# Performance work log

Hardware: AMD Instinct MI355X
Metric: run time of the kernel (lower is better)

The kernel has to match this reference:

```python
import jax, jax.numpy as jnp
import numpy as np

EPS = 1e-12


def pairwise_sqdist(x, y):
    # x: (B, N, 3), y: (B, M, 3) -> (B, N, M) squared euclidean distances
    xx = jnp.sum(x * x, axis=-1)              # (B, N)
    yy = jnp.sum(y * y, axis=-1)              # (B, M)
    xy = jnp.einsum('bnd,bmd->bnm', x, y)     # (B, N, M)
    d = xx[:, :, None] + yy[None_ if False else yy[:, None, :].shape and 0 or ...] if False else xx[:, :, None] + yy[:, None, :] - 2.0 * xy
    return jnp.maximum(d, 0.0)


def chamfer_l1(x, y):
    # pytorch3d/PoinTr-style ChamferDistanceL1:
    # mean over points of sqrt(min squared dist), averaged over both directions
    d = pairwise_sqdist(x, y)                 # (B, N, M)
    d1 = jnp.min(d, axis=2)                   # (B, N) x -> nearest y
    d2 = jnp.min(d, axis=1)                   # (B, M) y -> nearest x
    d1 = jnp.sqrt(jnp.maximum(d1, EPS))
    d2 = jnp.sqrt(jnp.maximum(d2, EPS))
    return 0.5 * (jnp.mean(d1) + jnp.mean(d2))


def knn1_gather(x, y):
    # For each point in x (B,N,3), find nearest neighbor in y (B,M,3) (K=1)
    # and gather it -> (B, N, 3). Matches knn_points + knn_gather + squeeze.
    d = pairwise_sqdist(x, y)                 # (B, N, M)
    idx = jnp.argmin(d, axis=2)               # (B, N) int
    return jnp.take_along_axis(y, idx[:, :, None], axis=1)  # (B, N, 3)


def volume_with_wedge(p):
    # wedge-product volume over consecutive point triples:
    # V = sum_i (p_i x p_{i+1}) . p_{i+2} / 6  -> (B,)
    c = jnp.cross(p[:, :-2, :], p[:, 1:-1, :])  # (B, N-2, 3)
    return jnp.sum(jnp.einsum('bnd,bnd->bn', c, p[:, 2:, :]), axis=-1) / 6.0


def setup_inputs() -> dict:
    key = jax.random.key(0)
    k1, k2, k3 = jax.random.split(key, 3)
    B, Nc, Nf, M = 2, 512, 8192, 8192
    return {
        'source_coarse': jax.random.normal(k1, (B, Nc, 3), dtype=jnp.float32),
        'source_fine': jax.random.normal(k2, (B, Nf, 3), dtype=jnp.float32),
        'target_points': jax.random.normal(k3, (B, M, 3), dtype=jnp.float32),
    }


def reference(source_coarse, source_fine, target_points):
    lambda_rot = lambda_ref = lambda_align = lambda_geo = 1.0
    B = source_fine.shape[0]
    axis = jnp.broadcast_to(jnp.array([0.0, 0.0, 1.0], dtype=source_fine.dtype), (B, 3))
    plane_normal = jnp.broadcast_to(jnp.array([0.0, 1.0, 0.0], dtype=source_fine.dtype), (B, 3))

    # KNN (K=1) gather of nearest target point for each fine source point
    new_target = knn1_gather(source_fine, target_points)  # (B, Nf, 3)

    # alignment (Chamfer L1) losses
    loss_align_coarse = chamfer_l1(source_coarse, target_points)
    loss_align_fine = chamfer_l1(source_fine, target_points)

    # rotational symmetry loss
    in_proj = jnp.einsum('bij,bj->bi', source_fine, axis)      # (B, Nf)
    re_proj = jnp.einsum('bij,bj->bi', new_target, axis)
    loss_rot = jnp.mean((jnp.linalg.norm(in_proj, axis=-1) - jnp.linalg.norm(re_proj, axis=-1)) ** 2)

    # reflectional symmetry loss
    pn = plane_normal / jnp.linalg.norm(plane_normal, axis=-1, keepdims=True)
    in_dist = jnp.einsum('bij,bj->bi', source_fine, pn)
    re_dist = jnp.einsum('bij,bj->bi', new_target, pn)
    loss_ref = jnp.mean((in_dist - re_dist) ** 2)

    # geometric consistency (wedge-product volume) loss
    loss_geo = jnp.mean((volume_with_wedge(source_fine) - volume_with_wedge(new_target)) ** 2)

    total = (lambda_rot * loss_rot + lambda_ref * loss_ref
             + lambda_align * loss_align_coarse + lambda_align * loss_align_fine
             + lambda_geo * loss_geo)
    return total
```

## Files before the change

kernel.cpp:

```cpp
#include <hip/hip_runtime.h>
#include <stdint.h>
#include <float.h>

using u64 = unsigned long long;
typedef float v2f __attribute__((ext_vector_type(2)));

constexpr int B_ = 2;
constexpr int NC = 512;
constexpr int NF = 8192;
constexpr int MT = 8192;

constexpr int TPB  = 256;
constexpr int RPB  = 512;
constexpr int TILE = 256;
constexpr int CF   = 16;
constexpr int TAIL_BLOCKS = 196;

#define DEVINL __device__ __forceinline__

template<bool ARGMIN, int R2>
DEVINL void pairmin_body(const float* __restrict__ P, const float* __restrict__ Q,
                         int nP, int nQ, int b, int row_base, int j0, int ntiles,
                         int chunk, int nRowsTot,
                         u64* __restrict__ outPack, unsigned* __restrict__ outVal,
                         float4* tile)
{
#pragma clang fp contract(off)
    const int tid = threadIdx.x;
    v2f tx0[R2], tx1[R2], tx2[R2], txx[R2], dbest[R2];
    int jb[2 * R2];
    #pragma unroll
    for (int r = 0; r < R2; ++r) {
        const int row0 = row_base + tid + (2 * r) * TPB;
        const int row1 = row_base + tid + (2 * r + 1) * TPB;
        const float* p0 = P + ((size_t)b * nP + row0) * 3;
        const float* p1 = P + ((size_t)b * nP + row1) * 3;
        float a0 = p0[0], a1 = p0[1], a2 = p0[2];
        float e0 = p1[0], e1 = p1[1], e2 = p1[2];
        tx0[r] = v2f{2.0f * a0, 2.0f * e0};
        tx1[r] = v2f{2.0f * a1, 2.0f * e1};
        tx2[r] = v2f{2.0f * a2, 2.0f * e2};
        txx[r] = v2f{(a0*a0 + a1*a1) + a2*a2, (e0*e0 + e1*e1) + e2*e2};
        dbest[r] = v2f{FLT_MAX, FLT_MAX};
        jb[2 * r] = 0; jb[2 * r + 1] = 0;
    }

    auto PROC = [&](const float4 qv, const int j) {
#pragma clang fp contract(off)
        #pragma unroll
        for (int r = 0; r < R2; ++r) {
            v2f s = (tx0[r] * qv.x + tx1[r] * qv.y) + tx2[r] * qv.z;
            v2f d = (txx[r] + qv.w) - s;
            if (ARGMIN) {
                bool c0 = d.x < dbest[r].x;
                bool c1 = d.y < dbest[r].y;
                dbest[r] = __builtin_elementwise_min(d, dbest[r]);
                jb[2 * r]     = c0 ? j : jb[2 * r];
                jb[2 * r + 1] = c1 ? j : jb[2 * r + 1];
            } else {
                dbest[r] = __builtin_elementwise_min(dbest[r], d);
            }
        }
    };

    {
        const float* q = Q + ((size_t)b * nQ + j0 + tid) * 3;
        float nq0 = q[0], nq1 = q[1], nq2 = q[2];

        for (int t = 0; t < ntiles; ++t) {
            __syncthreads();
            tile[tid] = make_float4(nq0, nq1, nq2, (nq0*nq0 + nq1*nq1) + nq2*nq2);
            if (t + 1 < ntiles) {
                const float* qn = Q + ((size_t)b * nQ + j0 + (t + 1) * TILE + tid) * 3;
                nq0 = qn[0]; nq1 = qn[1]; nq2 = qn[2];
            }
            __syncthreads();
            const int jbase = j0 + t * TILE;

            float4 qa[4], qb[4];
            #pragma unroll
            for (int u = 0; u < 4; ++u) qa[u] = tile[u];

            for (int jj = 0; jj < TILE; jj += 8) {
                #pragma unroll
                for (int u = 0; u < 4; ++u) qb[u] = tile[jj + 4 + u];
                #pragma unroll
                for (int u = 0; u < 4; ++u) PROC(qa[u], jbase + jj + u);
                #pragma unroll
                for (int u = 0; u < 4; ++u) qa[u] = tile[(jj + 8 + u) & (TILE - 1)];
                #pragma unroll
                for (int u = 0; u < 4; ++u) PROC(qb[u], jbase + jj + 4 + u);
            }
        }
    }

    const v2f vzero = {0.0f, 0.0f};
    const size_t o0 = (size_t)chunk * nRowsTot + (size_t)b * nP;
    #pragma unroll
    for (int r = 0; r < R2; ++r) {
        v2f dcl = __builtin_elementwise_max(dbest[r], vzero);
        const int row0 = row_base + tid + (2 * r) * TPB;
        const int row1 = row_base + tid + (2 * r + 1) * TPB;
        if (ARGMIN) {
            outPack[o0 + row0] = ((u64)__float_as_uint(dcl.x) << 32) | (unsigned)jb[2 * r];
            outPack[o0 + row1] = ((u64)__float_as_uint(dcl.y) << 32) | (unsigned)jb[2 * r + 1];
        } else {
            outVal[o0 + row0] = __float_as_uint(dcl.x);
            outVal[o0 + row1] = __float_as_uint(dcl.y);
        }
    }
}

__global__ __launch_bounds__(TPB, 4) void pairmin_all(
    const float* __restrict__ coarse, const float* __restrict__ fine,
    const float* __restrict__ tgt,
    u64* __restrict__ pfr, unsigned* __restrict__ pfc,
    unsigned* __restrict__ pcr, unsigned* __restrict__ pcc,
    unsigned* __restrict__ counter)
{
    __shared__ float4 tile[TILE];
    const int bx = blockIdx.x;
    if (bx == 0 && threadIdx.x == 0) *counter = 0;
    if (bx < 256) {
        int chunk = bx & 15, yb = (bx >> 4) & 7, b = bx >> 7;
        pairmin_body<true, 2>(fine, tgt, NF, MT, b, yb * 1024, chunk * (MT / CF), 2,
                              chunk, B_ * NF, pfr, nullptr, tile);
    } else if (bx < 512) {
        int i = bx - 256;
        int chunk = i & 15, yb = (i >> 4) & 7, b = i >> 7;
        pairmin_body<false, 2>(tgt, fine, MT, NF, b, yb * 1024, chunk * (NF / CF), 2,
                               chunk, B_ * MT, nullptr, pfc, tile);
    } else if (bx < 576) {
        int i = bx - 512;
        int chunk = i & 31, b = i >> 5;
        pairmin_body<false, 1>(coarse, tgt, NC, MT, b, 0, chunk * TILE, 1,
                               chunk, B_ * NC, nullptr, pcr, tile);
    } else {
        int i = bx - 576;
        int chunk = i & 1, yb = (i >> 1) & 15, b = i >> 5;
        pairmin_body<false, 1>(tgt, coarse, MT, NC, b, yb * RPB, chunk * TILE, 1,
                               chunk, B_ * MT, nullptr, pcc, tile);
    }
}

__global__ __launch_bounds__(TPB) void tail_all(
    const float* __restrict__ fine, const float* __restrict__ tgt,
    const u64* __restrict__ pfr, const unsigned* __restrict__ pfc,
    const unsigned* __restrict__ pcr, const unsigned* __restrict__ pcc,
    double* __restrict__ bs, unsigned* __restrict__ counter,
    float* __restrict__ out)
{
    __shared__ float sp[TPB + 2][3], yp[TPB + 2][3];
    __shared__ double redw[4][9];
    __shared__ double lred[4][13];
    __shared__ int lastflag;
    const int bx = blockIdx.x, tid = threadIdx.x;
    const int wave = tid >> 6, lane = tid & 63;

    double v_s = 0, v_d2f = 0, v_d1c = 0, v_d2c = 0, v_yd2 = 0, v_zs = 0, v_zt = 0;
    double vs = 0, vt = 0;
    int role_b = 0;

    if (bx < 64) {
        const int base = bx * TPB;
        const int g = base + tid;
        const int b = base >> 13;  role_b = b;
        u64 best = pfr[g];
        #pragma unroll
        for (int c = 1; c < CF; ++c) {
            u64 p = pfr[(size_t)c * (B_ * NF) + g];
            best = p < best ? p : best;
        }
        float d1 = __uint_as_float((unsigned)(best >> 32));
        int idx  = (int)(best & 0xffffffffULL);
        float s = sqrtf(fmaxf(d1, 1e-12f));
        const float* y  = tgt  + ((size_t)b * MT + idx) * 3;
        const float* sr = fine + (size_t)g * 3;
        float y0 = y[0],  y1 = y[1],  y2 = y[2];
        float s0 = sr[0], s1 = sr[1], s2 = sr[2];
        yp[tid][0] = y0; yp[tid][1] = y1; yp[tid][2] = y2;
        sp[tid][0] = s0; sp[tid][1] = s1; sp[tid][2] = s2;
        const int base_b = base & (NF - 1);
        if (tid < 2 && base_b + TPB + tid < NF) {
            int g2 = base + TPB + tid;
            u64 b2 = pfr[g2];
            #pragma unroll
            for (int c = 1; c < CF; ++c) {
                u64 p = pfr[(size_t)c * (B_ * NF) + g2];
                b2 = p < b2 ? p : b2;
            }
            int i2 = (int)(b2 & 0xffffffffULL);
            const float* yh = tgt  + ((size_t)b * MT + i2) * 3;
            const float* sh = fine + (size_t)g2 * 3;
            #pragma unroll
            for (int k = 0; k < 3; ++k) { yp[TPB + tid][k] = yh[k]; sp[TPB + tid][k] = sh[k]; }
        }
        __syncthreads();
        v_s = s;
        float yd = s1 - y1;
        v_yd2 = (double)(yd * yd);
        v_zs  = (double)(s2 * s2);
        v_zt  = (double)(y2 * y2);
        int rb = base_b + tid;
        if (rb <= NF - 3) {
            {
                const float* a = sp[tid]; const float* c = sp[tid+1]; const float* e = sp[tid+2];
                float c0 = a[1]*c[2] - a[2]*c[1];
                float c1 = a[2]*c[0] - a[0]*c[2];
                float c2 = a[0]*c[1] - a[1]*c[0];
                vs = (double)(c0*e[0] + c1*e[1] + c2*e[2]);
            }
            {
                const float* a = yp[tid]; const float* c = yp[tid+1]; const float* e = yp[tid+2];
                float c0 = a[1]*c[2] - a[2]*c[1];
                float c1 = a[2]*c[0] - a[0]*c[2];
                float c2 = a[0]*c[1] - a[1]*c[0];
                vt = (double)(c0*e[0] + c1*e[1] + c2*e[2]);
            }
        }
    } else if (bx < 128) {
        const int g = (bx - 64) * TPB + tid;
        unsigned best = pfc[g];
        #pragma unroll
        for (int c = 1; c < CF; ++c) best = min(best, pfc[(size_t)c * (B_ * MT) + g]);
        v_d2f = (double)sqrtf(fmaxf(__uint_as_float(best), 1e-12f));
    } else if (bx < 132) {
        const int g = (bx - 128) * TPB + tid;
        unsigned best = pcr[g];
        #pragma unroll
        for (int c = 1; c < 32; ++c) best = min(best, pcr[(size_t)c * (B_ * NC) + g]);
        v_d1c = (double)sqrtf(fmaxf(__uint_as_float(best), 1e-12f));
    } else {
        const int g = (bx - 132) * TPB + tid;
        unsigned best = min(pcc[g], pcc[(size_t)(B_ * MT) + g]);
        v_d2c = (double)sqrtf(fmaxf(__uint_as_float(best), 1e-12f));
    }

    double r9[9] = {v_s, v_d2f, v_d1c, v_d2c, v_yd2, v_zs, v_zt, vs, vt};
    for (int o = 32; o; o >>= 1) {
        #pragma unroll
        for (int k = 0; k < 9; ++k) r9[k] += __shfl_down(r9[k], o);
    }
    if (lane == 0) {
        #pragma unroll
        for (int k = 0; k < 9; ++k) redw[wave][k] = r9[k];
    }
    __syncthreads();
    if (tid == 0) {
        double t9[9];
        #pragma unroll
        for (int k = 0; k < 9; ++k)
            t9[k] = redw[0][k] + redw[1][k] + redw[2][k] + redw[3][k];
        double* o = bs + (size_t)bx * 16;
        #pragma unroll
        for (int k = 0; k < 16; ++k) o[k] = 0.0;
        o[0] = t9[0]; o[1] = t9[1]; o[2] = t9[2]; o[3] = t9[3]; o[4] = t9[4];
        o[5 + role_b]  = t9[5];
        o[7 + role_b]  = t9[6];
        o[9 + role_b]  = t9[7];
        o[11 + role_b] = t9[8];
        __threadfence();
        unsigned old = atomicAdd(counter, 1u);
        lastflag = (old == TAIL_BLOCKS - 1);
    }
    __syncthreads();
    if (!lastflag) return;

    __threadfence();
    double c13[13];
    if (tid < TAIL_BLOCKS) {
        const double* p = bs + (size_t)tid * 16;
        #pragma unroll
        for (int k = 0; k < 13; ++k) c13[k] = p[k];
    } else {
        #pragma unroll
        for (int k = 0; k < 13; ++k) c13[k] = 0.0;
    }
    for (int o = 32; o; o >>= 1) {
        #pragma unroll
        for (int k = 0; k < 13; ++k) c13[k] += __shfl_down(c13[k], o);
    }
    if (lane == 0) {
        #pragma unroll
        for (int k = 0; k < 13; ++k) lred[wave][k] = c13[k];
    }
    __syncthreads();
    if (tid == 0) {
        double S[13];
        #pragma unroll
        for (int k = 0; k < 13; ++k)
            S[k] = lred[0][k] + lred[1][k] + lred[2][k] + lred[3][k];
        double m_d1f = S[0] / (double)(B_ * NF);
        double m_d2f = S[1] / (double)(B_ * MT);
        double m_d1c = S[2] / (double)(B_ * NC);
        double m_d2c = S[3] / (double)(B_ * MT);
        double loss_align_fine   = 0.5 * (m_d1f + m_d2f);
        double loss_align_coarse = 0.5 * (m_d1c + m_d2c);
        double loss_ref = S[4] / (double)(B_ * NF);
        double loss_rot = 0.0, loss_geo = 0.0;
        for (int b = 0; b < B_; ++b) {
            double dn = sqrt(S[5 + b]) - sqrt(S[7 + b]);
            loss_rot += dn * dn;
            double dv = (S[9 + b] - S[11 + b]) / 6.0;
            loss_geo += dv * dv;
        }
        loss_rot /= (double)B_;
        loss_geo /= (double)B_;
        out[0] = (float)(loss_rot + loss_ref + loss_align_coarse + loss_align_fine + loss_geo);
    }
}

extern "C" void kernel_launch(void* const* d_in, const int* in_sizes, int n_in,
                              void* d_out, int out_size, void* d_ws, size_t ws_size,
                              hipStream_t stream)
{
    const float* src_coarse = (const float*)d_in[0];
    const float* src_fine   = (const float*)d_in[1];
    const float* tgt        = (const float*)d_in[2];
    float* out = (float*)d_out;
    char*  ws  = (char*)d_ws;

    u64*      pfr     = (u64*)(ws);
    unsigned* pfc     = (unsigned*)(ws + 2097152);
    unsigned* pcr     = (unsigned*)(ws + 3145728);
    unsigned* pcc     = (unsigned*)(ws + 3276800);
    double*   bs      = (double*)(ws + 3407872);
    unsigned* counter = (unsigned*)(ws + 3432960);

    pairmin_all<<<dim3(640), TPB, 0, stream>>>(
        src_coarse, src_fine, tgt, pfr, pfc, pcr, pcc, counter);
    tail_all<<<dim3(TAIL_BLOCKS), TPB, 0, stream>>>(
        src_fine, tgt, pfr, pfc, pcr, pcc, bs, counter, out);
}
```

Before: 117.5 us.

## Broadcast query points via readlane instead of LDS tiles and rebalance block work

Replaces the shared-memory tile of query points with per-wave register loading, using readlane to broadcast each point's coordinates across the wave. This removes __syncthreads and LDS traffic from the inner distance loop. Every block now runs both fine-direction phases plus one coarse phase, with the work split into more chunks (32/128/8), so the workspace and tail reductions grow. The scalar broadcasts may occupy the SALU and limit issue rate, and the argmin update changes from a vector min to per-lane selects.

After: 124.8 us. +6.2%, slower.

```diff
diff --git a/kernel.cpp b/kernel.cpp
--- a/kernel.cpp
+++ b/kernel.cpp
@@ -10,23 +10,28 @@
 constexpr int NF = 8192;
 constexpr int MT = 8192;
 
-constexpr int TPB  = 256;
-constexpr int RPB  = 512;
-constexpr int TILE = 256;
-constexpr int CF   = 16;
+constexpr int TPB = 256;
+constexpr int CFF = 32;
+constexpr int CCR = 128;
+constexpr int CCC = 8;
 constexpr int TAIL_BLOCKS = 196;
 
 #define DEVINL __device__ __forceinline__
 
+DEVINL float bcast(float v, int l) {
+    return __int_as_float(__builtin_amdgcn_readlane(__float_as_int(v), l));
+}
+
 template<bool ARGMIN, int R2>
-DEVINL void pairmin_body(const float* __restrict__ P, const float* __restrict__ Q,
-                         int nP, int nQ, int b, int row_base, int j0, int ntiles,
-                         int chunk, int nRowsTot,
-                         u64* __restrict__ outPack, unsigned* __restrict__ outVal,
-                         float4* tile)
+DEVINL void pairmin_phase(const float* __restrict__ P, const float* __restrict__ Q,
+                          int nP, int nQ, int b, int row_base, int j0, int ntiles,
+                          int chunk, int nRowsTot,
+                          u64* __restrict__ outPack, unsigned* __restrict__ outVal)
 {
 #pragma clang fp contract(off)
-    const int tid = threadIdx.x;
+    const int tid  = threadIdx.x;
+    const int lane = tid & 63;
+
     v2f tx0[R2], tx1[R2], tx2[R2], txx[R2], dbest[R2];
     int jb[2 * R2];
     #pragma unroll
@@ -45,53 +50,39 @@
         jb[2 * r] = 0; jb[2 * r + 1] = 0;
     }
 
-    auto PROC = [&](const float4 qv, const int j) {
-#pragma clang fp contract(off)
-        #pragma unroll
-        for (int r = 0; r < R2; ++r) {
-            v2f s = (tx0[r] * qv.x + tx1[r] * qv.y) + tx2[r] * qv.z;
-            v2f d = (txx[r] + qv.w) - s;
-            if (ARGMIN) {
-                bool c0 = d.x < dbest[r].x;
-                bool c1 = d.y < dbest[r].y;
-                dbest[r] = __builtin_elementwise_min(d, dbest[r]);
-                jb[2 * r]     = c0 ? j : jb[2 * r];
-                jb[2 * r + 1] = c1 ? j : jb[2 * r + 1];
-            } else {
-                dbest[r] = __builtin_elementwise_min(dbest[r], d);
+    const float* qp = Q + ((size_t)b * nQ + j0 + lane) * 3;
+    float cq0 = qp[0], cq1 = qp[1], cq2 = qp[2];
+
+    for (int t = 0; t < ntiles; ++t) {
+        float cqq = (cq0*cq0 + cq1*cq1) + cq2*cq2;
+        const int t2 = (t + 1 < ntiles) ? t + 1 : t;
+        const float* qn = Q + ((size_t)b * nQ + j0 + t2 * 64 + lane) * 3;
+        float nq0 = qn[0], nq1 = qn[1], nq2 = qn[2];
+        const int jbase = j0 + t * 64;
+
+        #pragma unroll
+        for (int l = 0; l < 64; ++l) {
+            const float q0 = bcast(cq0, l);
+            const float q1 = bcast(cq1, l);
+            const float q2 = bcast(cq2, l);
+            const float qq = bcast(cqq, l);
+            #pragma unroll
+            for (int r = 0; r < R2; ++r) {
+                v2f s = (tx0[r] * q0 + tx1[r] * q1) + tx2[r] * q2;
+                v2f d = (txx[r] + qq) - s;
+                if (ARGMIN) {
+                    bool c0 = d.x < dbest[r].x;
+                    bool c1 = d.y < dbest[r].y;
+                    dbest[r].x = c0 ? d.x : dbest[r].x;
+                    dbest[r].y = c1 ? d.y : dbest[r].y;
+                    jb[2 * r]     = c0 ? (jbase + l) : jb[2 * r];
+                    jb[2 * r + 1] = c1 ? (jbase + l) : jb[2 * r + 1];
+                } else {
+                    dbest[r] = __builtin_elementwise_min(dbest[r], d);
+                }
             }
         }
-    };
-
-    {
-        const float* q = Q + ((size_t)b * nQ + j0 + tid) * 3;
-        float nq0 = q[0], nq1 = q[1], nq2 = q[2];
-
-        for (int t = 0; t < ntiles; ++t) {
-            __syncthreads();
-            tile[tid] = make_float4(nq0, nq1, nq2, (nq0*nq0 + nq1*nq1) + nq2*nq2);
-            if (t + 1 < ntiles) {
-                const float* qn = Q + ((size_t)b * nQ + j0 + (t + 1) * TILE + tid) * 3;
-                nq0 = qn[0]; nq1 = qn[1]; nq2 = qn[2];
-            }
-            __syncthreads();
-            const int jbase = j0 + t * TILE;
-
-            float4 qa[4], qb[4];
-            #pragma unroll
-            for (int u = 0; u < 4; ++u) qa[u] = tile[u];
-
-            for (int jj = 0; jj < TILE; jj += 8) {
-                #pragma unroll
-                for (int u = 0; u < 4; ++u) qb[u] = tile[jj + 4 + u];
-                #pragma unroll
-                for (int u = 0; u < 4; ++u) PROC(qa[u], jbase + jj + u);
-                #pragma unroll
-                for (int u = 0; u < 4; ++u) qa[u] = tile[(jj + 8 + u) & (TILE - 1)];
-                #pragma unroll
-                for (int u = 0; u < 4; ++u) PROC(qb[u], jbase + jj + 4 + u);
-            }
-        }
+        cq0 = nq0; cq1 = nq1; cq2 = nq2;
     }
 
     const v2f vzero = {0.0f, 0.0f};
@@ -118,28 +109,26 @@
     unsigned* __restrict__ pcr, unsigned* __restrict__ pcc,
     unsigned* __restrict__ counter)
 {
-    __shared__ float4 tile[TILE];
     const int bx = blockIdx.x;
     if (bx == 0 && threadIdx.x == 0) *counter = 0;
-    if (bx < 256) {
-        int chunk = bx & 15, yb = (bx >> 4) & 7, b = bx >> 7;
-        pairmin_body<true, 2>(fine, tgt, NF, MT, b, yb * 1024, chunk * (MT / CF), 2,
-                              chunk, B_ * NF, pfr, nullptr, tile);
-    } else if (bx < 512) {
-        int i = bx - 256;
-        int chunk = i & 15, yb = (i >> 4) & 7, b = i >> 7;
-        pairmin_body<false, 2>(tgt, fine, MT, NF, b, yb * 1024, chunk * (NF / CF), 2,
-                               chunk, B_ * MT, nullptr, pfc, tile);
-    } else if (bx < 576) {
-        int i = bx - 512;
-        int chunk = i & 31, b = i >> 5;
-        pairmin_body<false, 1>(coarse, tgt, NC, MT, b, 0, chunk * TILE, 1,
-                               chunk, B_ * NC, nullptr, pcr, tile);
+    const int b   = bx >> 8;
+    const int sub = bx & 255;
+    const int g   = sub >> 5;
+    const int c   = sub & 31;
+
+    pairmin_phase<true, 2>(fine, tgt, NF, MT, b, g * 1024, c * 256, 4,
+                           c, B_ * NF, pfr, nullptr);
+    pairmin_phase<false, 2>(tgt, fine, MT, NF, b, g * 1024, c * 256, 4,
+                            c, B_ * MT, nullptr, pfc);
+    if (sub < 128) {
+        pairmin_phase<false, 1>(coarse, tgt, NC, MT, b, 0, sub * 64, 1,
+                                sub, B_ * NC, nullptr, pcr);
     } else {
-        int i = bx - 576;
-        int chunk = i & 1, yb = (i >> 1) & 15, b = i >> 5;
-        pairmin_body<false, 1>(tgt, coarse, MT, NC, b, yb * RPB, chunk * TILE, 1,
-                               chunk, B_ * MT, nullptr, pcc, tile);
+        const int s2 = sub - 128;
+        const int rg = s2 & 15;
+        const int jc = s2 >> 4;
+        pairmin_phase<false, 1>(tgt, coarse, MT, NC, b, rg * 512, jc * 64, 1,
+                                jc, B_ * MT, nullptr, pcc);
     }
 }
 
@@ -167,8 +156,8 @@
         const int b = base >> 13;  role_b = b;
         u64 best = pfr[g];
         #pragma unroll
-        for (int c = 1; c < CF; ++c) {
-            u64 p = pfr[(size_t)c * (B_ * NF) + g];
+        for (int cc = 1; cc < CFF; ++cc) {
+            u64 p = pfr[(size_t)cc * (B_ * NF) + g];
             best = p < best ? p : best;
         }
         float d1 = __uint_as_float((unsigned)(best >> 32));
@@ -185,8 +174,8 @@
             int g2 = base + TPB + tid;
             u64 b2 = pfr[g2];
             #pragma unroll
-            for (int c = 1; c < CF; ++c) {
-                u64 p = pfr[(size_t)c * (B_ * NF) + g2];
+            for (int cc = 1; cc < CFF; ++cc) {
+                u64 p = pfr[(size_t)cc * (B_ * NF) + g2];
                 b2 = p < b2 ? p : b2;
             }
             int i2 = (int)(b2 & 0xffffffffULL);
@@ -204,35 +193,36 @@
         int rb = base_b + tid;
         if (rb <= NF - 3) {
             {
-                const float* a = sp[tid]; const float* c = sp[tid+1]; const float* e = sp[tid+2];
-                float c0 = a[1]*c[2] - a[2]*c[1];
-                float c1 = a[2]*c[0] - a[0]*c[2];
-                float c2 = a[0]*c[1] - a[1]*c[0];
-                vs = (double)(c0*e[0] + c1*e[1] + c2*e[2]);
+                const float* a = sp[tid]; const float* c2 = sp[tid+1]; const float* e = sp[tid+2];
+                float c0 = a[1]*c2[2] - a[2]*c2[1];
+                float c1 = a[2]*c2[0] - a[0]*c2[2];
+                float c2v = a[0]*c2[1] - a[1]*c2[0];
+                vs = (double)(c0*e[0] + c1*e[1] + c2v*e[2]);
             }
             {
-                const float* a = yp[tid]; const float* c = yp[tid+1]; const float* e = yp[tid+2];
-                float c0 = a[1]*c[2] - a[2]*c[1];
-                float c1 = a[2]*c[0] - a[0]*c[2];
-                float c2 = a[0]*c[1] - a[1]*c[0];
-                vt = (double)(c0*e[0] + c1*e[1] + c2*e[2]);
+                const float* a = yp[tid]; const float* c2 = yp[tid+1]; const float* e = yp[tid+2];
+                float c0 = a[1]*c2[2] - a[2]*c2[1];
+                float c1 = a[2]*c2[0] - a[0]*c2[2];
+                float c2v = a[0]*c2[1] - a[1]*c2[0];
+                vt = (double)(c0*e[0] + c1*e[1] + c2v*e[2]);
             }
         }
     } else if (bx < 128) {
         const int g = (bx - 64) * TPB + tid;
         unsigned best = pfc[g];
         #pragma unroll
-        for (int c = 1; c < CF; ++c) best = min(best, pfc[(size_t)c * (B_ * MT) + g]);
+        for (int cc = 1; cc < CFF; ++cc) best = min(best, pfc[(size_t)cc * (B_ * MT) + g]);
         v_d2f = (double)sqrtf(fmaxf(__uint_as_float(best), 1e-12f));
     } else if (bx < 132) {
         const int g = (bx - 128) * TPB + tid;
         unsigned best = pcr[g];
-        #pragma unroll
-        for (int c = 1; c < 32; ++c) best = min(best, pcr[(size_t)c * (B_ * NC) + g]);
+        for (int cc = 1; cc < CCR; ++cc) best = min(best, pcr[(size_t)cc * (B_ * NC) + g]);
         v_d1c = (double)sqrtf(fmaxf(__uint_as_float(best), 1e-12f));
     } else {
         const int g = (bx - 132) * TPB + tid;
-        unsigned best = min(pcc[g], pcc[(size_t)(B_ * MT) + g]);
+        unsigned best = pcc[g];
+        #pragma unroll
+        for (int cc = 1; cc < CCC; ++cc) best = min(best, pcc[(size_t)cc * (B_ * MT) + g]);
         v_d2c = (double)sqrtf(fmaxf(__uint_as_float(best), 1e-12f));
     }
 
@@ -321,13 +311,13 @@
     char*  ws  = (char*)d_ws;
 
     u64*      pfr     = (u64*)(ws);
-    unsigned* pfc     = (unsigned*)(ws + 2097152);
-    unsigned* pcr     = (unsigned*)(ws + 3145728);
-    unsigned* pcc     = (unsigned*)(ws + 3276800);
-    double*   bs      = (double*)(ws + 3407872);
-    unsigned* counter = (unsigned*)(ws + 3432960);
-
-    pairmin_all<<<dim3(640), TPB, 0, stream>>>(
+    unsigned* pfc     = (unsigned*)(ws + 4194304);
+    unsigned* pcr     = (unsigned*)(ws + 6291456);
+    unsigned* pcc     = (unsigned*)(ws + 6815744);
+    double*   bs      = (double*)(ws + 7340032);
+    unsigned* counter = (unsigned*)(ws + 7365120);
+
+    pairmin_all<<<dim3(512), TPB, 0, stream>>>(
         src_coarse, src_fine, tgt, pfr, pfc, pcr, pcc, counter);
     tail_all<<<dim3(TAIL_BLOCKS), TPB, 0, stream>>>(
         src_fine, tgt, pfr, pfc, pcr, pcc, bs, counter, out);
```
